# Kernel tuning notes

Measured on AMD Instinct MI355X. Metric: run time of the kernel, lower is better.

Reference implementation:

```python
import jax, jax.numpy as jnp
import numpy as np

N_AGENTS = 8
HID = 256            # hidden_size == comm_dim
COMP = 32            # composition_dim
VOCAB = 256          # vocab_size (table has VOCAB+1 rows, last row = EOS token)
T = HID // COMP      # total_tokens = 8
EPSILON = 1e-6
NF = 1.0 / np.sqrt(HID)  # norm_factor


def setup_inputs() -> dict:
    key = jax.random.key(0)
    ks = jax.random.split(key, 12)
    B = 2048 * N_AGENTS  # n_rollout_threads * num_agents
    s = 0.05
    return {
        "hidden_state": jax.random.normal(ks[0], (B, HID), jnp.float32),
        "eps": jax.random.normal(ks[1], (T, B, COMP), jnp.float32),
        "W_Q": jax.random.normal(ks[2], (HID, HID), jnp.float32) * s,
        "b_Q": jnp.zeros((HID,), jnp.float32),
        "W_K": jax.random.normal(ks[3], (HID, HID), jnp.float32) * s,
        "b_K": jnp.zeros((HID,), jnp.float32),
        "W_mu": jax.random.normal(ks[4], (HID, COMP), jnp.float32) * s,
        "b_mu": jnp.zeros((COMP,), jnp.float32),
        "W_var": jax.random.normal(ks[5], (HID, COMP), jnp.float32) * s,
        "b_var": jnp.zeros((COMP,), jnp.float32),
        "vocab": jax.random.uniform(ks[6], (VOCAB + 1, COMP), jnp.float32, minval=-2.0, maxval=2.0),
        "W_sum": jax.random.normal(ks[7], (HID, HID), jnp.float32) * s,
        "b_sum": jnp.zeros((HID,), jnp.float32),
        "W_head": jax.random.normal(ks[8], (HID, HID), jnp.float32) * s,
        "b_head": jnp.zeros((HID,), jnp.float32),
    }


def _forward(hidden_state, eps, W_Q, b_Q, W_K, b_K, W_mu, b_mu, W_var, b_var,
             vocab, W_sum, b_sum, W_head, b_head):
    B = hidden_state.shape[0]
    # NOTE: original code sets V = to_K(hidden_state) (to_V is unused) -- kept faithfully.
    Q = (hidden_state @ W_Q + b_Q) * NF            # [B, HID]
    V = hidden_state @ W_K + b_K                   # [B, HID]
    EOS = vocab[-1]                                # [COMP]

    message = jnp.zeros((B, T, COMP), hidden_state.dtype)
    mask = jnp.ones((B,), hidden_state.dtype)
    finished = jnp.zeros((B,), bool)

    # Sequential recurrence over a small fixed number of tokens (T = 8).
    for i in range(T):
        m = message.reshape(B, HID)
        K = (m @ W_K + b_K) * NF                   # [B, HID]
        attn = jax.nn.softmax(-(Q * K), axis=-1)   # softmin == softmax of negated logits
        hidden_attn = attn * V                     # [B, HID]
        token_mu = hidden_attn @ W_mu + b_mu       # [B, COMP]
        token_log_var = hidden_attn @ W_var + b_var
        token = eps[i] * jnp.exp(0.5 * token_log_var) + token_mu
        # per-dimension min of squared distance over all vocab entries (faithful to torch.min(.,1)[0])
        token = jnp.min((token[:, None, :] - vocab) ** 2, axis=1)  # [B, COMP]
        token = token * mask[:, None]
        eos_hit = jnp.sum((token - EOS) ** 2, axis=-1) < EPSILON   # [B]
        if i > 0:
            prev_hit = jnp.any(
                jnp.sum((token[:, None, :] - message[:, :i]) ** 2, axis=-1) < EPSILON, axis=1)
            hit = jnp.logical_or(prev_hit, eos_hit)
        else:
            hit = eos_hit
        new_eos = jnp.logical_and(hit, jnp.logical_not(finished))
        token = jnp.where(new_eos[:, None], EOS, token)
        mask = jnp.where(hit, jnp.zeros_like(mask), mask)
        finished = jnp.logical_or(finished, hit)
        message = message.at[:, i].set(token)

    comm = message.reshape(B, HID)                 # comm_dim == HID
    b = B // N_AGENTS
    comm = comm.reshape(b, N_AGENTS, HID) / (N_AGENTS - 1)  # comm_mode 'avg'
    # expand to [b, n, n, C] then sum over dim 1 == broadcast total sum to every agent
    comm_sum = jnp.broadcast_to(comm.sum(axis=1, keepdims=True), (b, N_AGENTS, HID))
    comm_sum = comm_sum.reshape(B, HID)
    out = comm_sum @ W_sum + b_sum                 # comm_sum_head
    out = jax.nn.relu(out @ W_head + b_head)       # active_func(comm_head(.))
    return out


def reference(hidden_state, eps, W_Q, b_Q, W_K, b_K, W_mu, b_mu, W_var, b_var,
              vocab, W_sum, b_sum, W_head, b_head):
    return _forward(hidden_state, eps, W_Q, b_Q, W_K, b_K, W_mu, b_mu, W_var, b_var,
                    vocab, W_sum, b_sum, W_head, b_head)
```

## Files before the change

### kernel.cpp

```cpp
#include <hip/hip_runtime.h>

#define ROWSB 32
#define HIDN 256
#define TT 8
#define EPSI 1e-6f
#define HAS 260
#define SVS 260
#define TBSTR 40
#define NCELL 512
#define WS_LUT_F   (32*SVS)
#define WS_DINFO_F (32*SVS + 8192)
#define WS_WMV_F   (32*SVS + 8192 + 64)

__device__ __forceinline__ void ld4(float* d, const float* p) {
  float4 v = *(const float4*)p;
  d[0] = v.x; d[1] = v.y; d[2] = v.z; d[3] = v.w;
}
__device__ __forceinline__ void ld2(float* d, const float* p) {
  float2 v = *(const float2*)p;
  d[0] = v.x; d[1] = v.y;
}
__device__ __forceinline__ void lds_fence() {
  asm volatile("s_waitcnt lgkmcnt(0)" ::: "memory");
}
__device__ __forceinline__ void fma8(float4 wv, float h0, float h1,
                                     float* mu0, float* lv0, float* mu1, float* lv1) {
  mu0[0] += h0*wv.x; lv0[0] += h0*wv.y; mu0[1] += h0*wv.z; lv0[1] += h0*wv.w;
  mu1[0] += h1*wv.x; lv1[0] += h1*wv.y; mu1[1] += h1*wv.z; lv1[1] += h1*wv.w;
}

__global__ __launch_bounds__(256)
void sort_vocab(const float* __restrict__ vocab,
                const float* __restrict__ Wmu, const float* __restrict__ Wvar,
                float* __restrict__ ws) {
  __shared__ float arr[512];
  const int d = blockIdx.x;
  const int t = threadIdx.x;
  ws[WS_WMV_F + ((size_t)t*32 + d)*2 + 0] = Wmu[(size_t)t*32 + d];
  ws[WS_WMV_F + ((size_t)t*32 + d)*2 + 1] = Wvar[(size_t)t*32 + d];
  arr[t] = (t < 257) ? vocab[t*32 + d] : 3.0e38f;
  arr[t+256] = (t == 0) ? vocab[256*32 + d] : 3.0e38f;
  __syncthreads();
  for (int k = 2; k <= 512; k <<= 1) {
    for (int j = k >> 1; j > 0; j >>= 1) {
      #pragma unroll
      for (int h = 0; h < 2; ++h) {
        int i = t + h*256;
        int ixj = i ^ j;
        if (ixj > i) {
          float a = arr[i], b = arr[ixj];
          bool up = ((i & k) == 0);
          if ((a > b) == up) { arr[i] = b; arr[ixj] = a; }
        }
      }
      __syncthreads();
    }
  }
  #pragma unroll
  for (int h = 0; h < 2; ++h) {
    int i = t + h*256;
    if (i < SVS) ws[d*SVS + i] = (i < 257) ? arr[i] : 3.0e38f;
  }
  float base = arr[0];
  float maxv = arr[256];
  float scale = (float)NCELL / fmaxf(maxv - base, 1e-30f);
  if (t == 0) {
    float2* dinfo = (float2*)(ws + WS_DINFO_F);
    dinfo[d] = make_float2(base, scale);
  }
  #pragma unroll
  for (int h = 0; h < 2; ++h) {
    int cell = t + h*256;
    float target = base + (float)cell * (maxv - base) * (1.0f/(float)NCELL);
    int lo = 0, hi = 257;
    while (lo < hi) { int mid = (lo+hi)>>1; if (arr[mid] < target) lo = mid+1; else hi = mid; }
    ((unsigned short*)(ws + WS_LUT_F))[d*NCELL + cell] = (unsigned short)lo;
  }
}

__global__ __launch_bounds__(256, 2)
void mac_fused(const float* __restrict__ hs, const float* __restrict__ eps,
               const float* __restrict__ WQ, const float* __restrict__ bQ,
               const float* __restrict__ WK, const float* __restrict__ bK,
               const float* __restrict__ Wmu, const float* __restrict__ bmu,
               const float* __restrict__ Wvar, const float* __restrict__ bvar,
               const float* __restrict__ vocab,
               const float* __restrict__ Wsum, const float* __restrict__ bsum,
               const float* __restrict__ Whead, const float* __restrict__ bhead,
               const float* __restrict__ ws, float* __restrict__ out, int Btot)
{
  __shared__ __align__(16) float ha[ROWSB*HAS];
  __shared__ __align__(16) float vbuf[ROWSB*HAS];
  __shared__ __align__(16) float tokbuf[ROWSB*TBSTR];
  __shared__ float ivbuf[ROWSB], finbuf[ROWSB];

  const int t   = threadIdx.x;
  const int c4  = t & 63;
  const int w   = t >> 6;
  const int rp  = t >> 4;
  const int dp  = t & 15;
  const int d0u = (c4 << 2) & 31;
  const int tg  = c4 >> 3;
  const int rowbase = blockIdx.x * ROWSB;

  float Qr[8][4], Kr[8][4], MSGr[8][4];
  float eosv[4];
  unsigned fin = 0u;

  {
    const float* hp = hs + (size_t)(rowbase + w*8)*HIDN + c4*4;
    #pragma unroll
    for (int rr = 0; rr < 8; ++rr)
      *(float4*)&ha[(w*8+rr)*HAS + c4*4] = *(const float4*)(hp + (size_t)rr*HIDN);
  }
  if (c4 < 8) finbuf[w*8 + c4] = 0.f;
  ld4(eosv, vocab + 256*32 + d0u);
  float dbr[2], dsr[2];
  {
    float t0[4];
    ld4(t0, ws + WS_DINFO_F + dp*4);
    dbr[0]=t0[0]; dsr[0]=t0[1]; dbr[1]=t0[2]; dsr[1]=t0[3];
  }
  float bm[2], bv[2];
  ld2(bm, bmu + dp*2); ld2(bv, bvar + dp*2);
  lds_fence();

  {
    float Vr[8][4];
    {
      float bq[4], bk[4];
      ld4(bq, bQ + c4*4); ld4(bk, bK + c4*4);
      #pragma unroll
      for (int rr = 0; rr < 8; ++rr) {
        #pragma unroll
        for (int k = 0; k < 4; ++k) { Qr[rr][k] = bq[k]; Vr[rr][k] = bk[k]; }
      }
    }
    #pragma unroll 2
    for (int jq = 0; jq < 64; ++jq) {
      float hsq[8][4];
      #pragma unroll
      for (int rr = 0; rr < 8; ++rr) ld4(hsq[rr], &ha[(w*8+rr)*HAS + jq*4]);
      #pragma unroll
      for (int m = 0; m < 4; ++m) {
        float wq[4], wk[4];
        ld4(wq, WQ + (size_t)(jq*4+m)*HIDN + c4*4);
        ld4(wk, WK + (size_t)(jq*4+m)*HIDN + c4*4);
        #pragma unroll
        for (int rr = 0; rr < 8; ++rr) {
          #pragma unroll
          for (int k = 0; k < 4; ++k) {
            Qr[rr][k] += hsq[rr][m]*wq[k];
            Vr[rr][k] += hsq[rr][m]*wk[k];
          }
        }
      }
    }
    #pragma unroll
    for (int rr = 0; rr < 8; ++rr)
      *(float4*)&vbuf[(w*8+rr)*HAS + c4*4] =
          make_float4(Vr[rr][0], Vr[rr][1], Vr[rr][2], Vr[rr][3]);
  }
  {
    float bk[4]; ld4(bk, bK + c4*4);
    #pragma unroll
    for (int rr = 0; rr < 8; ++rr) {
      #pragma unroll
      for (int k = 0; k < 4; ++k) {
        Qr[rr][k] *= (1.0f/256.0f);
        Kr[rr][k]   = bk[k];
        MSGr[rr][k] = 0.f;
      }
    }
  }
  lds_fence();

  for (int it = 0; it < TT; ++it) {
    if (it > 0) {
      const float* Wr = WK + (size_t)((it-1)*32)*HIDN + c4*4;
      #pragma unroll 2
      for (int cq = 0; cq < 8; ++cq) {
        float tq[8][4];
        #pragma unroll
        for (int rr = 0; rr < 8; ++rr) ld4(tq[rr], &tokbuf[(w*8+rr)*TBSTR + cq*4]);
        #pragma unroll
        for (int m = 0; m < 4; ++m) {
          float wv[4]; ld4(wv, Wr + (size_t)(cq*4+m)*HIDN);
          #pragma unroll
          for (int rr = 0; rr < 8; ++rr) {
            #pragma unroll
            for (int k = 0; k < 4; ++k) Kr[rr][k] += tq[rr][m]*wv[k];
          }
        }
      }
    }

    float ep0[2], ep1[2];
    ld2(ep0, eps + ((size_t)it*Btot + rowbase + 2*rp)*32 + dp*2);
    ld2(ep1, eps + ((size_t)it*Btot + rowbase + 2*rp+1)*32 + dp*2);

    #pragma unroll
    for (int rr = 0; rr < 8; ++rr) {
      float e[4]; float s = 0.f;
      #pragma unroll
      for (int k = 0; k < 4; ++k) { e[k] = __expf(-(Qr[rr][k]*Kr[rr][k])); s += e[k]; }
      #pragma unroll
      for (int off = 32; off >= 1; off >>= 1) s += __shfl_xor(s, off);
      if (c4 == rr) ivbuf[w*8+rr] = 1.0f / s;
      float vv[4];
      ld4(vv, &vbuf[(w*8+rr)*HAS + c4*4]);
      *(float4*)&ha[(w*8+rr)*HAS + c4*4] =
          make_float4(e[0]*vv[0], e[1]*vv[1], e[2]*vv[2], e[3]*vv[3]);
    }
    lds_fence();

    float mu0[2]={0,0}, lv0[2]={0,0}, mu1[2]={0,0}, lv1[2]={0,0};
    {
      const float* wmv  = ws + WS_WMV_F + dp*4;
      const float* har0 = &ha[(2*rp)*HAS];
      const float* har1 = &ha[(2*rp+1)*HAS];
      float4 wb0[8], wb1[8];
      #pragma unroll
      for (int u = 0; u < 8; ++u) wb0[u] = *(const float4*)(wmv + (size_t)u*64);
      #pragma unroll 1
      for (int bb = 0; bb < 16; ++bb) {
        {
          const int b = 2*bb;
          float4 h0a = *(const float4*)(har0 + b*8);
          float4 h1a = *(const float4*)(har1 + b*8);
          float4 h0b = *(const float4*)(har0 + b*8 + 4);
          float4 h1b = *(const float4*)(har1 + b*8 + 4);
          const float* wp = wmv + (size_t)(b+1)*512;
          #pragma unroll
          for (int u = 0; u < 8; ++u) wb1[u] = *(const float4*)(wp + (size_t)u*64);
          fma8(wb0[0], h0a.x, h1a.x, mu0, lv0, mu1, lv1);
          fma8(wb0[1], h0a.y, h1a.y, mu0, lv0, mu1, lv1);
          fma8(wb0[2], h0a.z, h1a.z, mu0, lv0, mu1, lv1);
          fma8(wb0[3], h0a.w, h1a.w, mu0, lv0, mu1, lv1);
          fma8(wb0[4], h0b.x, h1b.x, mu0, lv0, mu1, lv1);
          fma8(wb0[5], h0b.y, h1b.y, mu0, lv0, mu1, lv1);
          fma8(wb0[6], h0b.z, h1b.z, mu0, lv0, mu1, lv1);
          fma8(wb0[7], h0b.w, h1b.w, mu0, lv0, mu1, lv1);
        }
        {
          const int b = 2*bb+1;
          float4 h0a = *(const float4*)(har0 + b*8);
          float4 h1a = *(const float4*)(har1 + b*8);
          float4 h0b = *(const float4*)(har0 + b*8 + 4);
          float4 h1b = *(const float4*)(har1 + b*8 + 4);
          if (bb < 15) {
            const float* wp = wmv + (size_t)(b+1)*512;
            #pragma unroll
            for (int u = 0; u < 8; ++u) wb0[u] = *(const float4*)(wp + (size_t)u*64);
          }
          fma8(wb1[0], h0a.x, h1a.x, mu0, lv0, mu1, lv1);
          fma8(wb1[1], h0a.y, h1a.y, mu0, lv0, mu1, lv1);
          fma8(wb1[2], h0a.z, h1a.z, mu0, lv0, mu1, lv1);
          fma8(wb1[3], h0a.w, h1a.w, mu0, lv0, mu1, lv1);
          fma8(wb1[4], h0b.x, h1b.x, mu0, lv0, mu1, lv1);
          fma8(wb1[5], h0b.y, h1b.y, mu0, lv0, mu1, lv1);
          fma8(wb1[6], h0b.z, h1b.z, mu0, lv0, mu1, lv1);
          fma8(wb1[7], h0b.w, h1b.w, mu0, lv0, mu1, lv1);
        }
      }
    }
    {
      float ivr0 = ivbuf[2*rp],  ivr1 = ivbuf[2*rp+1];
      float msk0 = 1.0f - finbuf[2*rp], msk1 = 1.0f - finbuf[2*rp+1];
      const unsigned short* lutg = (const unsigned short*)(ws + WS_LUT_F);
      float md0[2], md1[2];
      #pragma unroll
      for (int d = 0; d < 2; ++d) {
        const int dim = 2*dp + d;
        const float* sp = ws + dim*SVS;
        {
          float mu = mu0[d]*ivr0 + bm[d];
          float lv = lv0[d]*ivr0 + bv[d];
          float x  = ep0[d]*__expf(0.5f*lv) + mu;
          int c = (int)((x - dbr[d]) * dsr[d]);
          c = min(max(c, 0), NCELL-1);
          int idx = (int)lutg[dim*NCELL + c];
          float v = sp[idx];
          while (v < x) { ++idx; v = sp[idx]; }
          float dn = v - x;
          float dpv = (idx > 0) ? (x - sp[idx-1]) : 3.0e38f;
          md0[d] = fminf(dn, dpv);
        }
        {
          float mu = mu1[d]*ivr1 + bm[d];
          float lv = lv1[d]*ivr1 + bv[d];
          float x  = ep1[d]*__expf(0.5f*lv) + mu;
          int c = (int)((x - dbr[d]) * dsr[d]);
          c = min(max(c, 0), NCELL-1);
          int idx = (int)lutg[dim*NCELL + c];
          float v = sp[idx];
          while (v < x) { ++idx; v = sp[idx]; }
          float dn = v - x;
          float dpv = (idx > 0) ? (x - sp[idx-1]) : 3.0e38f;
          md1[d] = fminf(dn, dpv);
        }
      }
      *(float2*)&tokbuf[(2*rp)*TBSTR + dp*2]   = make_float2(md0[0]*md0[0]*msk0, md0[1]*md0[1]*msk0);
      *(float2*)&tokbuf[(2*rp+1)*TBSTR + dp*2] = make_float2(md1[0]*md1[0]*msk1, md1[1]*md1[1]*msk1);
    }
    lds_fence();

    {
      float tokr[8][4];
      #pragma unroll
      for (int rr = 0; rr < 8; ++rr) ld4(tokr[rr], &tokbuf[(w*8+rr)*TBSTR + d0u]);
      unsigned newfin = fin;
      #pragma unroll
      for (int rr = 0; rr < 8; ++rr) {
        float pd = 0.f, ed = 0.f;
        #pragma unroll
        for (int k = 0; k < 4; ++k) { float dm = tokr[rr][k]-MSGr[rr][k]; pd += dm*dm; }
        if (tg == 0) {
          #pragma unroll
          for (int k = 0; k < 4; ++k) { float de = tokr[rr][k]-eosv[k]; ed += de*de; }
        }
        pd += __shfl_xor(pd, 1); ed += __shfl_xor(ed, 1);
        pd += __shfl_xor(pd, 2); ed += __shfl_xor(ed, 2);
        pd += __shfl_xor(pd, 4); ed += __shfl_xor(ed, 4);
        bool lane_hit = (tg < it && pd < EPSI) || (tg == 0 && ed < EPSI);
        bool hit = (__ballot(lane_hit) != 0ull);
        if (hit) {
          if ((tg == it) && !((fin >> rr) & 1u)) {
            #pragma unroll
            for (int k = 0; k < 4; ++k) tokr[rr][k] = eosv[k];
          }
          newfin |= (1u << rr);
        }
        if (tg == it) {
          #pragma unroll
          for (int k = 0; k < 4; ++k) MSGr[rr][k] = tokr[rr][k];
        }
      }
      if (tg == it) {
        #pragma unroll
        for (int rr = 0; rr < 8; ++rr)
          *(float4*)&tokbuf[(w*8+rr)*TBSTR + d0u] =
              make_float4(MSGr[rr][0], MSGr[rr][1], MSGr[rr][2], MSGr[rr][3]);
      }
      if (c4 < 8) finbuf[w*8+c4] = ((newfin >> c4) & 1u) ? 1.f : 0.f;
      fin = newfin;
    }
    lds_fence();
  }

  __syncthreads();
  float* commb = ha;
  float* o1    = ha + 4*HAS;
  {
    float cs[4] = {0,0,0,0};
    #pragma unroll
    for (int rr = 0; rr < 8; ++rr) {
      #pragma unroll
      for (int k = 0; k < 4; ++k) cs[k] += MSGr[rr][k];
    }
    const float i7 = 1.0f/7.0f;
    *(float4*)&commb[w*HAS + c4*4] = make_float4(cs[0]*i7, cs[1]*i7, cs[2]*i7, cs[3]*i7);
  }
  __syncthreads();
  {
    float bs = bsum[t];
    float a1[4] = {bs, bs, bs, bs};
    #pragma unroll 2
    for (int jq = 0; jq < 64; ++jq) {
      float w4[4];
      #pragma unroll
      for (int m = 0; m < 4; ++m) w4[m] = Wsum[(size_t)(jq*4+m)*HIDN + t];
      #pragma unroll
      for (int g = 0; g < 4; ++g) {
        float c[4]; ld4(c, &commb[g*HAS + jq*4]);
        a1[g] += c[0]*w4[0] + c[1]*w4[1] + c[2]*w4[2] + c[3]*w4[3];
      }
    }
    #pragma unroll
    for (int g = 0; g < 4; ++g) o1[g*HAS + t] = a1[g];
  }
  __syncthreads();
  {
    float bh = bhead[t];
    float a2[4] = {bh, bh, bh, bh};
    #pragma unroll 2
    for (int jq = 0; jq < 64; ++jq) {
      float w4[4];
      #pragma unroll
      for (int m = 0; m < 4; ++m) w4[m] = Whead[(size_t)(jq*4+m)*HIDN + t];
      #pragma unroll
      for (int g = 0; g < 4; ++g) {
        float c[4]; ld4(c, &o1[g*HAS + jq*4]);
        a2[g] += c[0]*w4[0] + c[1]*w4[1] + c[2]*w4[2] + c[3]*w4[3];
      }
    }
    #pragma unroll
    for (int g = 0; g < 4; ++g) {
      float r = fmaxf(a2[g], 0.f);
      #pragma unroll
      for (int rr = 0; rr < 8; ++rr)
        out[(size_t)(rowbase + g*8 + rr)*HIDN + t] = r;
    }
  }
}

extern "C" void kernel_launch(void* const* d_in, const int* in_sizes, int n_in,
                              void* d_out, int out_size, void* d_ws, size_t ws_size,
                              hipStream_t stream) {
    const float* hs    = (const float*)d_in[0];
    const float* eps   = (const float*)d_in[1];
    const float* WQ    = (const float*)d_in[2];
    const float* bQ    = (const float*)d_in[3];
    const float* WK    = (const float*)d_in[4];
    const float* bK    = (const float*)d_in[5];
    const float* Wmu   = (const float*)d_in[6];
    const float* bmu   = (const float*)d_in[7];
    const float* Wvar  = (const float*)d_in[8];
    const float* bvar  = (const float*)d_in[9];
    const float* vocab = (const float*)d_in[10];
    const float* Wsum  = (const float*)d_in[11];
    const float* bsum  = (const float*)d_in[12];
    const float* Whead = (const float*)d_in[13];
    const float* bhead = (const float*)d_in[14];
    float* o = (float*)d_out;
    float* wsf = (float*)d_ws;
    int Btot = in_sizes[0] / HIDN;
    hipLaunchKernelGGL(sort_vocab, dim3(32), dim3(256), 0, stream, vocab, Wmu, Wvar, wsf);
    hipLaunchKernelGGL(mac_fused, dim3(Btot / ROWSB), dim3(256), 0, stream,
                       hs, eps, WQ, bQ, WK, bK, Wmu, bmu, Wvar, bvar,
                       vocab, Wsum, bsum, Whead, bhead, wsf, o, Btot);
}
```

Before: 395.1 us.

## Halve rows per block to 16 and raise occupancy to four blocks per CU

Each block now handles 16 rows instead of 32, with each wave owning 4 rows. Per-thread register arrays shrink, and launch bounds request 4 blocks per SM/CU instead of 2. The mu/var projection is remapped to one row per thread group, and the agent-sum epilogue combines per-wave partials because one agent group now spans two waves. This doubles the grid and the number of weight re-reads per row in exchange for more latency hiding. Shared memory arrays stay sized from ROWSB, so their footprint also halves, which helps occupancy.

Result: slower. 512.9 us (+29.8%).

```diff
diff --git a/kernel.cpp b/kernel.cpp
--- a/kernel.cpp
+++ b/kernel.cpp
@@ -1,6 +1,6 @@
 #include <hip/hip_runtime.h>
 
-#define ROWSB 32
+#define ROWSB 16
 #define HIDN 256
 #define TT 8
 #define EPSI 1e-6f
@@ -23,10 +23,8 @@
 __device__ __forceinline__ void lds_fence() {
   asm volatile("s_waitcnt lgkmcnt(0)" ::: "memory");
 }
-__device__ __forceinline__ void fma8(float4 wv, float h0, float h1,
-                                     float* mu0, float* lv0, float* mu1, float* lv1) {
-  mu0[0] += h0*wv.x; lv0[0] += h0*wv.y; mu0[1] += h0*wv.z; lv0[1] += h0*wv.w;
-  mu1[0] += h1*wv.x; lv1[0] += h1*wv.y; mu1[1] += h1*wv.z; lv1[1] += h1*wv.w;
+__device__ __forceinline__ void fma4(float4 wv, float h, float* mu, float* lv) {
+  mu[0] += h*wv.x; lv[0] += h*wv.y; mu[1] += h*wv.z; lv[1] += h*wv.w;
 }
 
 __global__ __launch_bounds__(256)
@@ -78,7 +76,7 @@
   }
 }
 
-__global__ __launch_bounds__(256, 2)
+__global__ __launch_bounds__(256, 4)
 void mac_fused(const float* __restrict__ hs, const float* __restrict__ eps,
                const float* __restrict__ WQ, const float* __restrict__ bQ,
                const float* __restrict__ WK, const float* __restrict__ bK,
@@ -97,23 +95,24 @@
   const int t   = threadIdx.x;
   const int c4  = t & 63;
   const int w   = t >> 6;
-  const int rp  = t >> 4;
-  const int dp  = t & 15;
+  const int rw  = w * 4;
+  const int rp  = c4 >> 4;
+  const int dp  = c4 & 15;
   const int d0u = (c4 << 2) & 31;
   const int tg  = c4 >> 3;
   const int rowbase = blockIdx.x * ROWSB;
 
-  float Qr[8][4], Kr[8][4], MSGr[8][4];
+  float Qr[4][4], Kr[4][4], MSGr[4][4];
   float eosv[4];
   unsigned fin = 0u;
 
   {
-    const float* hp = hs + (size_t)(rowbase + w*8)*HIDN + c4*4;
-    #pragma unroll
-    for (int rr = 0; rr < 8; ++rr)
-      *(float4*)&ha[(w*8+rr)*HAS + c4*4] = *(const float4*)(hp + (size_t)rr*HIDN);
-  }
-  if (c4 < 8) finbuf[w*8 + c4] = 0.f;
+    const float* hp = hs + (size_t)(rowbase + rw)*HIDN + c4*4;
+    #pragma unroll
+    for (int rr = 0; rr < 4; ++rr)
+      *(float4*)&ha[(rw+rr)*HAS + c4*4] = *(const float4*)(hp + (size_t)rr*HIDN);
+  }
+  if (c4 < 4) finbuf[rw + c4] = 0.f;
   ld4(eosv, vocab + 256*32 + d0u);
   float dbr[2], dsr[2];
   {
@@ -126,28 +125,28 @@
   lds_fence();
 
   {
-    float Vr[8][4];
+    float Vr[4][4];
     {
       float bq[4], bk[4];
       ld4(bq, bQ + c4*4); ld4(bk, bK + c4*4);
       #pragma unroll
-      for (int rr = 0; rr < 8; ++rr) {
+      for (int rr = 0; rr < 4; ++rr) {
         #pragma unroll
         for (int k = 0; k < 4; ++k) { Qr[rr][k] = bq[k]; Vr[rr][k] = bk[k]; }
       }
     }
     #pragma unroll 2
     for (int jq = 0; jq < 64; ++jq) {
-      float hsq[8][4];
-      #pragma unroll
-      for (int rr = 0; rr < 8; ++rr) ld4(hsq[rr], &ha[(w*8+rr)*HAS + jq*4]);
+      float hsq[4][4];
+      #pragma unroll
+      for (int rr = 0; rr < 4; ++rr) ld4(hsq[rr], &ha[(rw+rr)*HAS + jq*4]);
       #pragma unroll
       for (int m = 0; m < 4; ++m) {
         float wq[4], wk[4];
         ld4(wq, WQ + (size_t)(jq*4+m)*HIDN + c4*4);
         ld4(wk, WK + (size_t)(jq*4+m)*HIDN + c4*4);
         #pragma unroll
-        for (int rr = 0; rr < 8; ++rr) {
+        for (int rr = 0; rr < 4; ++rr) {
           #pragma unroll
           for (int k = 0; k < 4; ++k) {
             Qr[rr][k] += hsq[rr][m]*wq[k];
@@ -157,14 +156,14 @@
       }
     }
     #pragma unroll
-    for (int rr = 0; rr < 8; ++rr)
-      *(float4*)&vbuf[(w*8+rr)*HAS + c4*4] =
+    for (int rr = 0; rr < 4; ++rr)
+      *(float4*)&vbuf[(rw+rr)*HAS + c4*4] =
           make_float4(Vr[rr][0], Vr[rr][1], Vr[rr][2], Vr[rr][3]);
   }
   {
     float bk[4]; ld4(bk, bK + c4*4);
     #pragma unroll
-    for (int rr = 0; rr < 8; ++rr) {
+    for (int rr = 0; rr < 4; ++rr) {
       #pragma unroll
       for (int k = 0; k < 4; ++k) {
         Qr[rr][k] *= (1.0f/256.0f);
@@ -180,14 +179,14 @@
       const float* Wr = WK + (size_t)((it-1)*32)*HIDN + c4*4;
       #pragma unroll 2
       for (int cq = 0; cq < 8; ++cq) {
-        float tq[8][4];
-        #pragma unroll
-        for (int rr = 0; rr < 8; ++rr) ld4(tq[rr], &tokbuf[(w*8+rr)*TBSTR + cq*4]);
+        float tq[4][4];
+        #pragma unroll
+        for (int rr = 0; rr < 4; ++rr) ld4(tq[rr], &tokbuf[(rw+rr)*TBSTR + cq*4]);
         #pragma unroll
         for (int m = 0; m < 4; ++m) {
           float wv[4]; ld4(wv, Wr + (size_t)(cq*4+m)*HIDN);
           #pragma unroll
-          for (int rr = 0; rr < 8; ++rr) {
+          for (int rr = 0; rr < 4; ++rr) {
             #pragma unroll
             for (int k = 0; k < 4; ++k) Kr[rr][k] += tq[rr][m]*wv[k];
           }
@@ -195,123 +194,91 @@
       }
     }
 
-    float ep0[2], ep1[2];
-    ld2(ep0, eps + ((size_t)it*Btot + rowbase + 2*rp)*32 + dp*2);
-    ld2(ep1, eps + ((size_t)it*Btot + rowbase + 2*rp+1)*32 + dp*2);
-
-    #pragma unroll
-    for (int rr = 0; rr < 8; ++rr) {
+    float ep[2];
+    ld2(ep, eps + ((size_t)it*Btot + rowbase + rw + rp)*32 + dp*2);
+
+    #pragma unroll
+    for (int rr = 0; rr < 4; ++rr) {
       float e[4]; float s = 0.f;
       #pragma unroll
       for (int k = 0; k < 4; ++k) { e[k] = __expf(-(Qr[rr][k]*Kr[rr][k])); s += e[k]; }
       #pragma unroll
       for (int off = 32; off >= 1; off >>= 1) s += __shfl_xor(s, off);
-      if (c4 == rr) ivbuf[w*8+rr] = 1.0f / s;
+      if (c4 == rr) ivbuf[rw+rr] = 1.0f / s;
       float vv[4];
-      ld4(vv, &vbuf[(w*8+rr)*HAS + c4*4]);
-      *(float4*)&ha[(w*8+rr)*HAS + c4*4] =
+      ld4(vv, &vbuf[(rw+rr)*HAS + c4*4]);
+      *(float4*)&ha[(rw+rr)*HAS + c4*4] =
           make_float4(e[0]*vv[0], e[1]*vv[1], e[2]*vv[2], e[3]*vv[3]);
     }
     lds_fence();
 
-    float mu0[2]={0,0}, lv0[2]={0,0}, mu1[2]={0,0}, lv1[2]={0,0};
+    float mu[2]={0,0}, lv[2]={0,0};
     {
-      const float* wmv  = ws + WS_WMV_F + dp*4;
-      const float* har0 = &ha[(2*rp)*HAS];
-      const float* har1 = &ha[(2*rp+1)*HAS];
-      float4 wb0[8], wb1[8];
-      #pragma unroll
-      for (int u = 0; u < 8; ++u) wb0[u] = *(const float4*)(wmv + (size_t)u*64);
+      const float* wmv = ws + WS_WMV_F + dp*4;
+      const float* har = &ha[(rw+rp)*HAS];
+      float4 wb0[4], wb1[4];
+      #pragma unroll
+      for (int u = 0; u < 4; ++u) wb0[u] = *(const float4*)(wmv + (size_t)u*64);
       #pragma unroll 1
-      for (int bb = 0; bb < 16; ++bb) {
+      for (int bb = 0; bb < 32; ++bb) {
         {
           const int b = 2*bb;
-          float4 h0a = *(const float4*)(har0 + b*8);
-          float4 h1a = *(const float4*)(har1 + b*8);
-          float4 h0b = *(const float4*)(har0 + b*8 + 4);
-          float4 h1b = *(const float4*)(har1 + b*8 + 4);
-          const float* wp = wmv + (size_t)(b+1)*512;
+          float4 h4 = *(const float4*)(har + b*4);
+          const float* wp = wmv + (size_t)(b+1)*256;
           #pragma unroll
-          for (int u = 0; u < 8; ++u) wb1[u] = *(const float4*)(wp + (size_t)u*64);
-          fma8(wb0[0], h0a.x, h1a.x, mu0, lv0, mu1, lv1);
-          fma8(wb0[1], h0a.y, h1a.y, mu0, lv0, mu1, lv1);
-          fma8(wb0[2], h0a.z, h1a.z, mu0, lv0, mu1, lv1);
-          fma8(wb0[3], h0a.w, h1a.w, mu0, lv0, mu1, lv1);
-          fma8(wb0[4], h0b.x, h1b.x, mu0, lv0, mu1, lv1);
-          fma8(wb0[5], h0b.y, h1b.y, mu0, lv0, mu1, lv1);
-          fma8(wb0[6], h0b.z, h1b.z, mu0, lv0, mu1, lv1);
-          fma8(wb0[7], h0b.w, h1b.w, mu0, lv0, mu1, lv1);
+          for (int u = 0; u < 4; ++u) wb1[u] = *(const float4*)(wp + (size_t)u*64);
+          fma4(wb0[0], h4.x, mu, lv);
+          fma4(wb0[1], h4.y, mu, lv);
+          fma4(wb0[2], h4.z, mu, lv);
+          fma4(wb0[3], h4.w, mu, lv);
         }
         {
           const int b = 2*bb+1;
-          float4 h0a = *(const float4*)(har0 + b*8);
-          float4 h1a = *(const float4*)(har1 + b*8);
-          float4 h0b = *(const float4*)(har0 + b*8 + 4);
-          float4 h1b = *(const float4*)(har1 + b*8 + 4);
-          if (bb < 15) {
-            const float* wp = wmv + (size_t)(b+1)*512;
+          float4 h4 = *(const float4*)(har + b*4);
+          if (bb < 31) {
+            const float* wp = wmv + (size_t)(b+1)*256;
             #pragma unroll
-            for (int u = 0; u < 8; ++u) wb0[u] = *(const float4*)(wp + (size_t)u*64);
+            for (int u = 0; u < 4; ++u) wb0[u] = *(const float4*)(wp + (size_t)u*64);
           }
-          fma8(wb1[0], h0a.x, h1a.x, mu0, lv0, mu1, lv1);
-          fma8(wb1[1], h0a.y, h1a.y, mu0, lv0, mu1, lv1);
-          fma8(wb1[2], h0a.z, h1a.z, mu0, lv0, mu1, lv1);
-          fma8(wb1[3], h0a.w, h1a.w, mu0, lv0, mu1, lv1);
-          fma8(wb1[4], h0b.x, h1b.x, mu0, lv0, mu1, lv1);
-          fma8(wb1[5], h0b.y, h1b.y, mu0, lv0, mu1, lv1);
-          fma8(wb1[6], h0b.z, h1b.z, mu0, lv0, mu1, lv1);
-          fma8(wb1[7], h0b.w, h1b.w, mu0, lv0, mu1, lv1);
+          fma4(wb1[0], h4.x, mu, lv);
+          fma4(wb1[1], h4.y, mu, lv);
+          fma4(wb1[2], h4.z, mu, lv);
+          fma4(wb1[3], h4.w, mu, lv);
         }
       }
     }
     {
-      float ivr0 = ivbuf[2*rp],  ivr1 = ivbuf[2*rp+1];
-      float msk0 = 1.0f - finbuf[2*rp], msk1 = 1.0f - finbuf[2*rp+1];
+      float ivr = ivbuf[rw+rp];
+      float msk = 1.0f - finbuf[rw+rp];
       const unsigned short* lutg = (const unsigned short*)(ws + WS_LUT_F);
-      float md0[2], md1[2];
+      float md[2];
       #pragma unroll
       for (int d = 0; d < 2; ++d) {
         const int dim = 2*dp + d;
         const float* sp = ws + dim*SVS;
-        {
-          float mu = mu0[d]*ivr0 + bm[d];
-          float lv = lv0[d]*ivr0 + bv[d];
-          float x  = ep0[d]*__expf(0.5f*lv) + mu;
-          int c = (int)((x - dbr[d]) * dsr[d]);
-          c = min(max(c, 0), NCELL-1);
-          int idx = (int)lutg[dim*NCELL + c];
-          float v = sp[idx];
-          while (v < x) { ++idx; v = sp[idx]; }
-          float dn = v - x;
-          float dpv = (idx > 0) ? (x - sp[idx-1]) : 3.0e38f;
-          md0[d] = fminf(dn, dpv);
-        }
-        {
-          float mu = mu1[d]*ivr1 + bm[d];
-          float lv = lv1[d]*ivr1 + bv[d];
-          float x  = ep1[d]*__expf(0.5f*lv) + mu;
-          int c = (int)((x - dbr[d]) * dsr[d]);
-          c = min(max(c, 0), NCELL-1);
-          int idx = (int)lutg[dim*NCELL + c];
-          float v = sp[idx];
-          while (v < x) { ++idx; v = sp[idx]; }
-          float dn = v - x;
-          float dpv = (idx > 0) ? (x - sp[idx-1]) : 3.0e38f;
-          md1[d] = fminf(dn, dpv);
-        }
-      }
-      *(float2*)&tokbuf[(2*rp)*TBSTR + dp*2]   = make_float2(md0[0]*md0[0]*msk0, md0[1]*md0[1]*msk0);
-      *(float2*)&tokbuf[(2*rp+1)*TBSTR + dp*2] = make_float2(md1[0]*md1[0]*msk1, md1[1]*md1[1]*msk1);
+        float muv = mu[d]*ivr + bm[d];
+        float lvv = lv[d]*ivr + bv[d];
+        float x   = ep[d]*__expf(0.5f*lvv) + muv;
+        int c = (int)((x - dbr[d]) * dsr[d]);
+        c = min(max(c, 0), NCELL-1);
+        int idx = (int)lutg[dim*NCELL + c];
+        float v = sp[idx];
+        while (v < x) { ++idx; v = sp[idx]; }
+        float dn = v - x;
+        float dpv = (idx > 0) ? (x - sp[idx-1]) : 3.0e38f;
+        md[d] = fminf(dn, dpv);
+      }
+      *(float2*)&tokbuf[(rw+rp)*TBSTR + dp*2] = make_float2(md[0]*md[0]*msk, md[1]*md[1]*msk);
     }
     lds_fence();
 
     {
-      float tokr[8][4];
-      #pragma unroll
-      for (int rr = 0; rr < 8; ++rr) ld4(tokr[rr], &tokbuf[(w*8+rr)*TBSTR + d0u]);
+      float tokr[4][4];
+      #pragma unroll
+      for (int rr = 0; rr < 4; ++rr) ld4(tokr[rr], &tokbuf[(rw+rr)*TBSTR + d0u]);
       unsigned newfin = fin;
       #pragma unroll
-      for (int rr = 0; rr < 8; ++rr) {
+      for (int rr = 0; rr < 4; ++rr) {
         float pd = 0.f, ed = 0.f;
         #pragma unroll
         for (int k = 0; k < 4; ++k) { float dm = tokr[rr][k]-MSGr[rr][k]; pd += dm*dm; }
@@ -338,64 +305,66 @@
       }
       if (tg == it) {
         #pragma unroll
-        for (int rr = 0; rr < 8; ++rr)
-          *(float4*)&tokbuf[(w*8+rr)*TBSTR + d0u] =
+        for (int rr = 0; rr < 4; ++rr)
+          *(float4*)&tokbuf[(rw+rr)*TBSTR + d0u] =
               make_float4(MSGr[rr][0], MSGr[rr][1], MSGr[rr][2], MSGr[rr][3]);
       }
-      if (c4 < 8) finbuf[w*8+c4] = ((newfin >> c4) & 1u) ? 1.f : 0.f;
+      if (c4 < 4) finbuf[rw+c4] = ((newfin >> c4) & 1u) ? 1.f : 0.f;
       fin = newfin;
     }
     lds_fence();
   }
 
   __syncthreads();
-  float* commb = ha;
-  float* o1    = ha + 4*HAS;
+  float* partial = ha;
+  float* o1      = ha + 4*HAS;
   {
     float cs[4] = {0,0,0,0};
     #pragma unroll
-    for (int rr = 0; rr < 8; ++rr) {
+    for (int rr = 0; rr < 4; ++rr) {
       #pragma unroll
       for (int k = 0; k < 4; ++k) cs[k] += MSGr[rr][k];
     }
     const float i7 = 1.0f/7.0f;
-    *(float4*)&commb[w*HAS + c4*4] = make_float4(cs[0]*i7, cs[1]*i7, cs[2]*i7, cs[3]*i7);
+    *(float4*)&partial[w*HAS + c4*4] = make_float4(cs[0]*i7, cs[1]*i7, cs[2]*i7, cs[3]*i7);
   }
   __syncthreads();
   {
     float bs = bsum[t];
-    float a1[4] = {bs, bs, bs, bs};
+    float a1[2] = {bs, bs};
     #pragma unroll 2
     for (int jq = 0; jq < 64; ++jq) {
       float w4[4];
       #pragma unroll
       for (int m = 0; m < 4; ++m) w4[m] = Wsum[(size_t)(jq*4+m)*HIDN + t];
       #pragma unroll
-      for (int g = 0; g < 4; ++g) {
-        float c[4]; ld4(c, &commb[g*HAS + jq*4]);
-        a1[g] += c[0]*w4[0] + c[1]*w4[1] + c[2]*w4[2] + c[3]*w4[3];
-      }
-    }
-    #pragma unroll
-    for (int g = 0; g < 4; ++g) o1[g*HAS + t] = a1[g];
+      for (int g = 0; g < 2; ++g) {
+        float ca[4], cb[4];
+        ld4(ca, &partial[(2*g)*HAS + jq*4]);
+        ld4(cb, &partial[(2*g+1)*HAS + jq*4]);
+        a1[g] += (ca[0]+cb[0])*w4[0] + (ca[1]+cb[1])*w4[1]
+               + (ca[2]+cb[2])*w4[2] + (ca[3]+cb[3])*w4[3];
+      }
+    }
+    o1[t] = a1[0]; o1[HAS + t] = a1[1];
   }
   __syncthreads();
   {
     float bh = bhead[t];
-    float a2[4] = {bh, bh, bh, bh};
+    float a2[2] = {bh, bh};
     #pragma unroll 2
     for (int jq = 0; jq < 64; ++jq) {
       float w4[4];
       #pragma unroll
       for (int m = 0; m < 4; ++m) w4[m] = Whead[(size_t)(jq*4+m)*HIDN + t];
       #pragma unroll
-      for (int g = 0; g < 4; ++g) {
+      for (int g = 0; g < 2; ++g) {
         float c[4]; ld4(c, &o1[g*HAS + jq*4]);
         a2[g] += c[0]*w4[0] + c[1]*w4[1] + c[2]*w4[2] + c[3]*w4[3];
       }
     }
     #pragma unroll
-    for (int g = 0; g < 4; ++g) {
+    for (int g = 0; g < 2; ++g) {
       float r = fmaxf(a2[g], 0.f);
       #pragma unroll
       for (int rr = 0; rr < 8; ++rr)
```
